# Optimization experiments

Hardware: AMD Instinct MI355X
Metric: run time of the kernel (lower is better)

## Reference

```python
import jax, jax.numpy as jnp
import numpy as np

B, N, T, D, H, E = 32768, 2, 4, 256, 8, 2
HD = D // H
S = N * T  # flattened seq_len = num_nodes * history_length
SCALE = 1.0 / np.sqrt(HD)


def setup_inputs() -> dict:
    key = jax.random.key(0)
    ks = jax.random.split(key, 22)

    def w(k, i, o):
        return jax.random.normal(k, (i, o), jnp.float32) * 0.02

    def b(k, o):
        return jax.random.normal(k, (o,), jnp.float32) * 0.01

    return {
        'node_features': jax.random.normal(ks[0], (B, N, T, D), jnp.float32),
        'edge_features': jax.random.normal(ks[1], (B, E), jnp.float32),
        'Wq': w(ks[2], D, D), 'bq': b(ks[3], D),
        'Wk': w(ks[4], D, D), 'bk': b(ks[5], D),
        'Wv': w(ks[6], D, D), 'bv': b(ks[7], D),
        'Wo': w(ks[8], D, D), 'bo': b(ks[9], D),
        'Wbias': w(ks[10], E, H), 'bbias': b(ks[11], H),
        'Wgate': w(ks[12], E, D), 'bgate': b(ks[13], D),
        'Wscale': w(ks[14], E, D), 'bscale': b(ks[15], D),
        'Wshift': w(ks[16], E, D), 'bshift': b(ks[17], D),
        'Whs': w(ks[18], E, H), 'bhs': b(ks[19], H),
    }


def reference(node_features, edge_features, Wq, bq, Wk, bk, Wv, bv, Wo, bo,
              Wbias, bbias, Wgate, bgate, Wscale, bscale, Wshift, bshift, Whs, bhs):
    # temporal mode: [B, N, T, D] -> [B, S, D]
    x = node_features.reshape(B, S, D)
    e = edge_features  # [B, E]

    Q = x @ Wq + bq
    K = x @ Wk + bk
    V = x @ Wv + bv

    # Edge-Conditioned Modulation of V
    gate = jax.nn.sigmoid(e @ Wgate + bgate)   # [B, D]
    scale = jnp.tanh(e @ Wscale + bscale)       # [B, D]
    shift = e @ Wshift + bshift                 # [B, D]
    V = (V * (1.0 + scale[:, None, :]) + shift[:, None, :]) * gate[:, None, :]

    # [B, H, S, HD]
    Qh = Q.reshape(B, S, H, HD).transpose(0, 2, 1, 3)
    Kh = K.reshape(B, S, H, HD).transpose(0, 2, 1, 3)
    Vh = V.reshape(B, S, H, HD).transpose(0, 2, 1, 3)

    scores = jnp.einsum('bhsd,bhtd->bhst', Qh, Kh) * SCALE  # [B, H, S, S]

    edge_bias = e @ Wbias + bbias                 # [B, H]
    head_scale = jnp.tanh(e @ Whs + bhs)          # [B, H]
    scores = scores * (1.0 + head_scale[:, :, None, None])

    # sparse temporal bias: (ee_t, obj_t) and (obj_t, ee_t) pairs only
    ee = jnp.arange(T)
    obj = T + ee
    bias = jnp.zeros((B, H, S, S), scores.dtype)
    bias = bias.at[:, :, ee, obj].set(edge_bias[:, :, None])
    bias = bias.at[:, :, obj, ee].set(edge_bias[:, :, None])
    scores = scores + bias

    attn = jax.nn.softmax(scores, axis=-1)  # dropout is identity in eval
    out = jnp.einsum('bhst,bhtd->bhsd', attn, Vh)  # [B, H, S, HD]
    out = out.transpose(0, 2, 1, 3).reshape(B, N, T, D).mean(axis=2)  # temporal pooling
    out = out @ Wo + bo  # [B, N, D]
    return out
```

## Files before the change

### kernel.cpp

```cpp
#include <hip/hip_runtime.h>


typedef short bf16x8 __attribute__((ext_vector_type(8)));
typedef float f32x4 __attribute__((ext_vector_type(4)));
typedef unsigned short u16;

#define SCALE_F 0.17677669529663687f
#define WT_BYTES (1024 * 256 * 2)

__device__ __forceinline__ float bf2f(u16 h) {
  unsigned u = ((unsigned)h) << 16; float f; __builtin_memcpy(&f, &u, 4); return f;
}
__device__ __forceinline__ u16 f2bf(float f) {
  unsigned u; __builtin_memcpy(&u, &f, 4);
  u += 0x7FFFu + ((u >> 16) & 1u);
  return (u16)(u >> 16);
}
__device__ __forceinline__ float fast_tanh(float x) {
  float e = __expf(2.0f * x);
  return (e - 1.0f) / (e + 1.0f);
}

template<bool F32>
__device__ __forceinline__ float LD(const void* p, int i) {
  if constexpr (F32) return ((const float*)p)[i];
  else return bf2f(((const u16*)p)[i]);
}

template<bool F32>
__device__ __forceinline__ bf16x8 load8bf_nt(const void* p, int idx) {
  if constexpr (F32) {
    const f32x4* f = (const f32x4*)((const float*)p + idx);
    f32x4 a = __builtin_nontemporal_load(f);
    f32x4 b = __builtin_nontemporal_load(f + 1);
    bf16x8 r;
    r[0] = (short)f2bf(a[0]); r[1] = (short)f2bf(a[1]);
    r[2] = (short)f2bf(a[2]); r[3] = (short)f2bf(a[3]);
    r[4] = (short)f2bf(b[0]); r[5] = (short)f2bf(b[1]);
    r[6] = (short)f2bf(b[2]); r[7] = (short)f2bf(b[3]);
    return r;
  } else {
    return __builtin_nontemporal_load((const bf16x8*)((const u16*)p + idx));
  }
}

__device__ __forceinline__ void gl_lds16(const u16* g, u16* l) {
  __builtin_amdgcn_global_load_lds(
      (const __attribute__((address_space(1))) unsigned int*)g,
      (__attribute__((address_space(3))) unsigned int*)l, 16, 0, 0);
}

__global__ void prep_kernel(const u16* __restrict__ x16,
                            const void* __restrict__ Wq, const void* __restrict__ Wk,
                            const void* __restrict__ Wv, const void* __restrict__ Wo,
                            int* __restrict__ flag, u16* __restrict__ WT) {
  __shared__ int tot;
  if (threadIdx.x == 0) tot = 0;
  __syncthreads();
  int cnt = 0;
  for (int i = threadIdx.x; i < 4096; i += 256) {
    int e = (x16[2 * i] >> 7) & 0xFF;
    cnt += (e >= 0x90 || e <= 0x50) ? 1 : 0;
  }
  atomicAdd(&tot, cnt);
  __syncthreads();
  const bool f32 = (tot >= 64);
  if (blockIdx.x == 0 && threadIdx.x == 0) *flag = f32 ? 1 : 0;

  int n = blockIdx.x;
  int k = threadIdx.x;
  if (n < 768) {
    int sel = n >> 8, col = n & 255;
    const void* src = sel == 0 ? Wq : (sel == 1 ? Wk : Wv);
    float v = f32 ? ((const float*)src)[k * 256 + col] : bf2f(((const u16*)src)[k * 256 + col]);
    WT[n * 256 + (k ^ ((n & 7) << 3))] = f2bf(v);
  } else {
    int col = n - 768;
    float v = f32 ? ((const float*)Wo)[k * 256 + col] : bf2f(((const u16*)Wo)[k * 256 + col]);
    WT[768 * 256 + col * 256 + k] = f2bf(v);
  }
}

struct __align__(16) Scratch {
  u16 qk[4][32][72];
  u16 vt[4][32][56];
  u16 pb[4][16][40];
};
union SharedU {
  u16 wtile[2][6144];
  Scratch s;
};

template<bool F32>
__device__ __forceinline__ void fused_impl(
    SharedU& sm,
    const void* __restrict__ x, const void* __restrict__ edge,
    const void* __restrict__ bq, const void* __restrict__ bk, const void* __restrict__ bv,
    const void* __restrict__ Wbias, const void* __restrict__ bbias,
    const void* __restrict__ Wgate, const void* __restrict__ bgate,
    const void* __restrict__ Wscale, const void* __restrict__ bscale,
    const void* __restrict__ Wshift, const void* __restrict__ bshift,
    const void* __restrict__ Whs, const void* __restrict__ bhs,
    const u16* __restrict__ WT, float* __restrict__ out) {
  const int tid = threadIdx.x;
  const int w  = tid >> 6;
  const int l  = tid & 63;
  const int ln = l & 15;
  const int q4 = l >> 4;
  u16* poolg = (u16*)out;

  {
    u16* vz = &sm.s.vt[w][0][0];
#pragma unroll
    for (int i = 0; i < 28; ++i) vz[l + 64 * i] = 0;
    u16* pz = &sm.s.pb[w][0][0];
#pragma unroll
    for (int i = 0; i < 10; ++i) pz[l + 64 * i] = 0;
  }

  float eA[4], eB[4];
#pragma unroll
  for (int i = 0; i < 4; ++i) {
    int gb = blockIdx.x * 16 + w * 4 + i;
    eA[i] = LD<F32>(edge, gb * 2);
    eB[i] = LD<F32>(edge, gb * 2 + 1);
  }

  const int xbase = (blockIdx.x * 128 + w * 32) * 256;
  bf16x8 xa[2][8];
#pragma unroll
  for (int mt = 0; mt < 2; ++mt)
#pragma unroll
    for (int ks = 0; ks < 8; ++ks)
      xa[mt][ks] = load8bf_nt<F32>(x, xbase + (mt * 16 + ln) * 256 + ks * 32 + q4 * 8);

  const u16* wsrc[3];
#pragma unroll
  for (int i = 0; i < 3; ++i) {
    int r = i * 32 + w * 8 + (l >> 3);
    int ngb = ((r >> 5) << 8) + (r & 31);
    wsrc[i] = WT + ngb * 256 + (l & 7) * 8;
  }
  int rowoff[6];
#pragma unroll
  for (int nt = 0; nt < 6; ++nt)
    rowoff[nt] = ((nt >> 1) * 32 + (nt & 1) * 16 + ln) * 64;
  const int swz = (ln & 7) << 3;

#pragma unroll 1
  for (int h = 0; h < 8; ++h) {
    f32x4 acc[2][6];
#pragma unroll
    for (int mt = 0; mt < 2; ++mt)
#pragma unroll
      for (int nt = 0; nt < 6; ++nt) acc[mt][nt] = (f32x4){0.f, 0.f, 0.f, 0.f};

    __syncthreads();
#pragma unroll
    for (int i = 0; i < 3; ++i)
      gl_lds16(wsrc[i] + h * 8192, &sm.wtile[0][(i * 32 + w * 8) * 64]);
    __syncthreads();
#pragma unroll
    for (int q = 0; q < 4; ++q) {
      if (q < 3) {
#pragma unroll
        for (int i = 0; i < 3; ++i)
          gl_lds16(wsrc[i] + h * 8192 + (q + 1) * 64,
                   &sm.wtile[(q + 1) & 1][(i * 32 + w * 8) * 64]);
      }
#pragma unroll
      for (int k2 = 0; k2 < 2; ++k2) {
        int cx = (k2 * 32 + q4 * 8) ^ swz;
        const u16* wq = &sm.wtile[q & 1][0];
#pragma unroll
        for (int nt = 0; nt < 6; ++nt) {
          bf16x8 bfr = *(const bf16x8*)(wq + rowoff[nt] + cx);
          acc[0][nt] = __builtin_amdgcn_mfma_f32_16x16x32_bf16(xa[0][q * 2 + k2], bfr, acc[0][nt], 0, 0, 0);
          acc[1][nt] = __builtin_amdgcn_mfma_f32_16x16x32_bf16(xa[1][q * 2 + k2], bfr, acc[1][nt], 0, 0, 0);
        }
      }
      __syncthreads();
    }

#pragma unroll
    for (int nt = 0; nt < 4; ++nt) {
      int cb = (nt & 1) * 16 + ln;
      float bias = LD<F32>((nt >> 1) ? bk : bq, h * 32 + cb);
      int col = (nt >> 1) * 32 + cb;
#pragma unroll
      for (int mt = 0; mt < 2; ++mt)
#pragma unroll
        for (int r = 0; r < 4; ++r)
          sm.s.qk[w][mt * 16 + q4 * 4 + r][col] = f2bf(acc[mt][nt][r] + bias);
    }
#pragma unroll
    for (int nt = 4; nt < 6; ++nt) {
      int dg = h * 32 + (nt - 4) * 16 + ln;
      float bvv = LD<F32>(bv, dg);
      float wg0 = LD<F32>(Wgate, dg),  wg1 = LD<F32>(Wgate, 256 + dg),  bg  = LD<F32>(bgate, dg);
      float ws0 = LD<F32>(Wscale, dg), ws1 = LD<F32>(Wscale, 256 + dg), bs  = LD<F32>(bscale, dg);
      float wf0 = LD<F32>(Wshift, dg), wf1 = LD<F32>(Wshift, 256 + dg), bsh = LD<F32>(bshift, dg);
#pragma unroll
      for (int mt = 0; mt < 2; ++mt) {
        float e0 = (q4 & 2) ? eA[mt * 2 + 1] : eA[mt * 2];
        float e1 = (q4 & 2) ? eB[mt * 2 + 1] : eB[mt * 2];
        float ga = 1.f / (1.f + __expf(-(e0 * wg0 + e1 * wg1 + bg)));
        float sc = fast_tanh(e0 * ws0 + e1 * ws1 + bs);
        float sh = e0 * wf0 + e1 * wf1 + bsh;
        u16 vv[4];
#pragma unroll
        for (int r = 0; r < 4; ++r) {
          float v = acc[mt][nt][r] + bvv;
          v = (v * (1.f + sc) + sh) * ga;
          vv[r] = f2bf(v);
        }
        ushort4 pk; pk.x = vv[0]; pk.y = vv[1]; pk.z = vv[2]; pk.w = vv[3];
        *(ushort4*)&sm.s.vt[w][(nt - 4) * 16 + ln][mt * 16 + q4 * 4] = pk;
      }
    }
    __asm__ volatile("" ::: "memory");

    float wb0 = LD<F32>(Wbias, h), wb1 = LD<F32>(Wbias, 8 + h), bb  = LD<F32>(bbias, h);
    float wh0 = LD<F32>(Whs, h),   wh1 = LD<F32>(Whs, 8 + h),   bh_ = LD<F32>(bhs, h);
#pragma unroll
    for (int pair = 0; pair < 2; ++pair) {
      bf16x8 qa = *(const bf16x8*)&sm.s.qk[w][pair * 16 + ln][q4 * 8];
      bf16x8 kb = *(const bf16x8*)&sm.s.qk[w][pair * 16 + ln][32 + q4 * 8];
      f32x4 z4 = {0.f, 0.f, 0.f, 0.f};
      f32x4 s = __builtin_amdgcn_mfma_f32_16x16x32_bf16(qa, kb, z4, 0, 0, 0);

      float e00 = eA[pair * 2],     e01 = eB[pair * 2];
      float e10 = eA[pair * 2 + 1], e11 = eB[pair * 2 + 1];
      float eb0 = e00 * wb0 + e01 * wb1 + bb;
      float eb1 = e10 * wb0 + e11 * wb1 + bb;
      float hs0 = fast_tanh(e00 * wh0 + e01 * wh1 + bh_);
      float hs1 = fast_tanh(e10 * wh0 + e11 * wh1 + bh_);
      int bj = ln >> 3;
      float mult = SCALE_F * (1.f + (bj ? hs1 : hs0));
      float ebias = bj ? eb1 : eb0;
      int tl = ln & 7;
      bool valid = ((q4 >> 1) == bj);
      float p[4];
#pragma unroll
      for (int r = 0; r < 4; ++r) {
        int sl = (q4 & 1) * 4 + r;
        p[r] = s[r] * mult + ((tl == (sl ^ 4)) ? ebias : 0.f);
      }
#pragma unroll
      for (int r = 0; r < 4; ++r) {
        float m = p[r];
        m = fmaxf(m, __shfl_xor(m, 1));
        m = fmaxf(m, __shfl_xor(m, 2));
        m = fmaxf(m, __shfl_xor(m, 4));
        float e = __expf(p[r] - m);
        float su = e;
        su += __shfl_xor(su, 1);
        su += __shfl_xor(su, 2);
        su += __shfl_xor(su, 4);
        p[r] = e / su;
      }
#pragma unroll
      for (int r = 0; r < 4; ++r)
        sm.s.pb[w][q4 * 4 + r][ln] = valid ? f2bf(p[r]) : (u16)0;
      __asm__ volatile("" ::: "memory");

      bf16x8 pa = *(const bf16x8*)&sm.s.pb[w][ln][q4 * 8];
#pragma unroll
      for (int nt = 0; nt < 2; ++nt) {
        bf16x8 vb = *(const bf16x8*)&sm.s.vt[w][nt * 16 + ln][pair * 16 + q4 * 8];
        f32x4 z = {0.f, 0.f, 0.f, 0.f};
        f32x4 o = __builtin_amdgcn_mfma_f32_16x16x32_bf16(pa, vb, z, 0, 0, 0);
        float pm = (o[0] + o[1] + o[2] + o[3]) * 0.25f;
        int c = w * 32 + h * 4 + pair * 2 + nt;
        poolg[(blockIdx.x * 32 + (c >> 2)) * 512 + 256 + (c & 3) * 64 + l] = f2bf(pm);
      }
    }
  }
}

__global__ __launch_bounds__(256, 4) void fused_kernel(
    const void* __restrict__ x, const void* __restrict__ edge,
    const void* __restrict__ bq, const void* __restrict__ bk, const void* __restrict__ bv,
    const void* __restrict__ Wbias, const void* __restrict__ bbias,
    const void* __restrict__ Wgate, const void* __restrict__ bgate,
    const void* __restrict__ Wscale, const void* __restrict__ bscale,
    const void* __restrict__ Wshift, const void* __restrict__ bshift,
    const void* __restrict__ Whs, const void* __restrict__ bhs,
    const int* __restrict__ flag, const u16* __restrict__ WT, float* __restrict__ out) {
  __shared__ SharedU sm;
  if (*flag)
    fused_impl<true>(sm, x, edge, bq, bk, bv, Wbias, bbias, Wgate, bgate,
                     Wscale, bscale, Wshift, bshift, Whs, bhs, WT, out);
  else
    fused_impl<false>(sm, x, edge, bq, bk, bv, Wbias, bbias, Wgate, bgate,
                      Wscale, bscale, Wshift, bshift, Whs, bhs, WT, out);
}

__global__ __launch_bounds__(256, 4) void proj_kernel(const void* __restrict__ bo,
                                                      const int* __restrict__ flag,
                                                      const u16* __restrict__ WT,
                                                      float* __restrict__ out) {
  __shared__ u16 pooled[32][264];
  const bool f32 = (*flag != 0);
  const int tid = threadIdx.x;
  const int w  = tid >> 6;
  const int l  = tid & 63;
  const int ln = l & 15;
  const int q4 = l >> 4;
  const u16* pool = (const u16*)out;
  const u16* WoT = WT + 768 * 256;
  const int rbase = blockIdx.x * 32;

#pragma unroll
  for (int i = 0; i < 32; ++i) {
    int idx = i * 256 + tid;
    int c = idx >> 6, lq = idx & 63;
    u16 v = pool[(rbase + (c >> 2)) * 512 + 256 + (c & 3) * 64 + lq];
    int wsrc = c >> 5, hh = (c >> 2) & 7, pr = (c >> 1) & 1, ntt = c & 1;
    int q4l = lq >> 4, lnl = lq & 15;
    int prow = wsrc * 8 + (pr * 2 + (q4l >> 1)) * 2 + (q4l & 1);
    pooled[prow][hh * 32 + ntt * 16 + lnl] = v;
  }
  __syncthreads();

  f32x4 fo[2][4];
#pragma unroll
  for (int mt = 0; mt < 2; ++mt)
#pragma unroll
    for (int nt = 0; nt < 4; ++nt) fo[mt][nt] = (f32x4){0.f, 0.f, 0.f, 0.f};
#pragma unroll
  for (int ks = 0; ks < 8; ++ks) {
    bf16x8 af0 = *(const bf16x8*)&pooled[ln][ks * 32 + q4 * 8];
    bf16x8 af1 = *(const bf16x8*)&pooled[16 + ln][ks * 32 + q4 * 8];
#pragma unroll
    for (int ntw = 0; ntw < 4; ++ntw) {
      int nrow = w * 64 + ntw * 16 + ln;
      bf16x8 bfr = *(const bf16x8*)(WoT + nrow * 256 + ks * 32 + q4 * 8);
      fo[0][ntw] = __builtin_amdgcn_mfma_f32_16x16x32_bf16(af0, bfr, fo[0][ntw], 0, 0, 0);
      fo[1][ntw] = __builtin_amdgcn_mfma_f32_16x16x32_bf16(af1, bfr, fo[1][ntw], 0, 0, 0);
    }
  }
#pragma unroll
  for (int ntw = 0; ntw < 4; ++ntw) {
    int col = w * 64 + ntw * 16 + ln;
    float bias = f32 ? ((const float*)bo)[col] : bf2f(((const u16*)bo)[col]);
#pragma unroll
    for (int mt = 0; mt < 2; ++mt)
#pragma unroll
      for (int r = 0; r < 4; ++r) {
        int row = mt * 16 + q4 * 4 + r;
        __builtin_nontemporal_store(fo[mt][ntw][r] + bias,
                                    &out[(rbase + row) * 256 + col]);
      }
  }
}

extern "C" void kernel_launch(void* const* d_in, const int* in_sizes, int n_in,
                              void* d_out, int out_size, void* d_ws, size_t ws_size,
                              hipStream_t stream) {
  (void)in_sizes; (void)n_in; (void)out_size; (void)ws_size;
  const void* x      = d_in[0];
  const void* edge   = d_in[1];
  const void* Wq     = d_in[2];  const void* bq  = d_in[3];
  const void* Wk     = d_in[4];  const void* bk  = d_in[5];
  const void* Wv     = d_in[6];  const void* bv  = d_in[7];
  const void* Wo     = d_in[8];  const void* bo  = d_in[9];
  const void* Wbias  = d_in[10]; const void* bbias  = d_in[11];
  const void* Wgate  = d_in[12]; const void* bgate  = d_in[13];
  const void* Wscale = d_in[14]; const void* bscale = d_in[15];
  const void* Wshift = d_in[16]; const void* bshift = d_in[17];
  const void* Whs    = d_in[18]; const void* bhs    = d_in[19];
  u16* WT   = (u16*)d_ws;
  int* flag = (int*)((char*)d_ws + WT_BYTES);
  float* out = (float*)d_out;

  prep_kernel<<<1024, 256, 0, stream>>>((const u16*)x, Wq, Wk, Wv, Wo, flag, WT);
  fused_kernel<<<2048, 256, 0, stream>>>(x, edge, bq, bk, bv, Wbias, bbias,
                                         Wgate, bgate, Wscale, bscale, Wshift, bshift,
                                         Whs, bhs, flag, WT, out);
  proj_kernel<<<2048, 256, 0, stream>>>(bo, flag, WT, out);
}
```

Before: 736.3 us.

## Fuse output projection into attention kernel, accumulating per head

```diff
diff --git a/kernel.cpp b/kernel.cpp
--- a/kernel.cpp
+++ b/kernel.cpp
@@ -85,6 +85,7 @@
   u16 qk[4][32][72];
   u16 vt[4][32][56];
   u16 pb[4][16][40];
+  u16 ps[32][40];
 };
 union SharedU {
   u16 wtile[2][6144];
@@ -96,6 +97,7 @@
     SharedU& sm,
     const void* __restrict__ x, const void* __restrict__ edge,
     const void* __restrict__ bq, const void* __restrict__ bk, const void* __restrict__ bv,
+    const void* __restrict__ bo,
     const void* __restrict__ Wbias, const void* __restrict__ bbias,
     const void* __restrict__ Wgate, const void* __restrict__ bgate,
     const void* __restrict__ Wscale, const void* __restrict__ bscale,
@@ -107,7 +109,7 @@
   const int l  = tid & 63;
   const int ln = l & 15;
   const int q4 = l >> 4;
-  u16* poolg = (u16*)out;
+  const u16* WoT = WT + 768 * 256;
 
   {
     u16* vz = &sm.s.vt[w][0][0];
@@ -146,6 +148,12 @@
   for (int nt = 0; nt < 6; ++nt)
     rowoff[nt] = ((nt >> 1) * 32 + (nt & 1) * 16 + ln) * 64;
   const int swz = (ln & 7) << 3;
+
+  f32x4 fo[2][4];
+#pragma unroll
+  for (int mt = 0; mt < 2; ++mt)
+#pragma unroll
+    for (int nt = 0; nt < 4; ++nt) fo[mt][nt] = (f32x4){0.f, 0.f, 0.f, 0.f};
 
 #pragma unroll 1
   for (int h = 0; h < 8; ++h) {
@@ -181,6 +189,11 @@
       }
       __syncthreads();
     }
+
+    bf16x8 wob[4];
+#pragma unroll
+    for (int ntw = 0; ntw < 4; ++ntw)
+      wob[ntw] = *(const bf16x8*)(WoT + (w * 64 + ntw * 16 + ln) * 256 + h * 32 + q4 * 8);
 
 #pragma unroll
     for (int nt = 0; nt < 4; ++nt) {
@@ -271,16 +284,41 @@
         f32x4 z = {0.f, 0.f, 0.f, 0.f};
         f32x4 o = __builtin_amdgcn_mfma_f32_16x16x32_bf16(pa, vb, z, 0, 0, 0);
         float pm = (o[0] + o[1] + o[2] + o[3]) * 0.25f;
-        int c = w * 32 + h * 4 + pair * 2 + nt;
-        poolg[(blockIdx.x * 32 + (c >> 2)) * 512 + 256 + (c & 3) * 64 + l] = f2bf(pm);
-      }
-    }
+        int prow = w * 8 + (pair * 2 + (q4 >> 1)) * 2 + (q4 & 1);
+        sm.s.ps[prow][nt * 16 + ln] = f2bf(pm);
+      }
+    }
+
+    __syncthreads();
+    {
+      bf16x8 pa0 = *(const bf16x8*)&sm.s.ps[ln][q4 * 8];
+      bf16x8 pa1 = *(const bf16x8*)&sm.s.ps[16 + ln][q4 * 8];
+#pragma unroll
+      for (int ntw = 0; ntw < 4; ++ntw) {
+        fo[0][ntw] = __builtin_amdgcn_mfma_f32_16x16x32_bf16(pa0, wob[ntw], fo[0][ntw], 0, 0, 0);
+        fo[1][ntw] = __builtin_amdgcn_mfma_f32_16x16x32_bf16(pa1, wob[ntw], fo[1][ntw], 0, 0, 0);
+      }
+    }
+  }
+
+#pragma unroll
+  for (int ntw = 0; ntw < 4; ++ntw) {
+    int col = w * 64 + ntw * 16 + ln;
+    float bias = LD<F32>(bo, col);
+#pragma unroll
+    for (int mt = 0; mt < 2; ++mt)
+#pragma unroll
+      for (int r = 0; r < 4; ++r) {
+        int row = mt * 16 + q4 * 4 + r;
+        out[(blockIdx.x * 32 + row) * 256 + col] = fo[mt][ntw][r] + bias;
+      }
   }
 }
 
 __global__ __launch_bounds__(256, 4) void fused_kernel(
     const void* __restrict__ x, const void* __restrict__ edge,
     const void* __restrict__ bq, const void* __restrict__ bk, const void* __restrict__ bv,
+    const void* __restrict__ bo,
     const void* __restrict__ Wbias, const void* __restrict__ bbias,
     const void* __restrict__ Wgate, const void* __restrict__ bgate,
     const void* __restrict__ Wscale, const void* __restrict__ bscale,
@@ -289,70 +327,11 @@
     const int* __restrict__ flag, const u16* __restrict__ WT, float* __restrict__ out) {
   __shared__ SharedU sm;
   if (*flag)
-    fused_impl<true>(sm, x, edge, bq, bk, bv, Wbias, bbias, Wgate, bgate,
+    fused_impl<true>(sm, x, edge, bq, bk, bv, bo, Wbias, bbias, Wgate, bgate,
                      Wscale, bscale, Wshift, bshift, Whs, bhs, WT, out);
   else
-    fused_impl<false>(sm, x, edge, bq, bk, bv, Wbias, bbias, Wgate, bgate,
+    fused_impl<false>(sm, x, edge, bq, bk, bv, bo, Wbias, bbias, Wgate, bgate,
                       Wscale, bscale, Wshift, bshift, Whs, bhs, WT, out);
-}
-
-__global__ __launch_bounds__(256, 4) void proj_kernel(const void* __restrict__ bo,
-                                                      const int* __restrict__ flag,
-                                                      const u16* __restrict__ WT,
-                                                      float* __restrict__ out) {
-  __shared__ u16 pooled[32][264];
-  const bool f32 = (*flag != 0);
-  const int tid = threadIdx.x;
-  const int w  = tid >> 6;
-  const int l  = tid & 63;
-  const int ln = l & 15;
-  const int q4 = l >> 4;
-  const u16* pool = (const u16*)out;
-  const u16* WoT = WT + 768 * 256;
-  const int rbase = blockIdx.x * 32;
-
-#pragma unroll
-  for (int i = 0; i < 32; ++i) {
-    int idx = i * 256 + tid;
-    int c = idx >> 6, lq = idx & 63;
-    u16 v = pool[(rbase + (c >> 2)) * 512 + 256 + (c & 3) * 64 + lq];
-    int wsrc = c >> 5, hh = (c >> 2) & 7, pr = (c >> 1) & 1, ntt = c & 1;
-    int q4l = lq >> 4, lnl = lq & 15;
-    int prow = wsrc * 8 + (pr * 2 + (q4l >> 1)) * 2 + (q4l & 1);
-    pooled[prow][hh * 32 + ntt * 16 + lnl] = v;
-  }
-  __syncthreads();
-
-  f32x4 fo[2][4];
-#pragma unroll
-  for (int mt = 0; mt < 2; ++mt)
-#pragma unroll
-    for (int nt = 0; nt < 4; ++nt) fo[mt][nt] = (f32x4){0.f, 0.f, 0.f, 0.f};
-#pragma unroll
-  for (int ks = 0; ks < 8; ++ks) {
-    bf16x8 af0 = *(const bf16x8*)&pooled[ln][ks * 32 + q4 * 8];
-    bf16x8 af1 = *(const bf16x8*)&pooled[16 + ln][ks * 32 + q4 * 8];
-#pragma unroll
-    for (int ntw = 0; ntw < 4; ++ntw) {
-      int nrow = w * 64 + ntw * 16 + ln;
-      bf16x8 bfr = *(const bf16x8*)(WoT + nrow * 256 + ks * 32 + q4 * 8);
-      fo[0][ntw] = __builtin_amdgcn_mfma_f32_16x16x32_bf16(af0, bfr, fo[0][ntw], 0, 0, 0);
-      fo[1][ntw] = __builtin_amdgcn_mfma_f32_16x16x32_bf16(af1, bfr, fo[1][ntw], 0, 0, 0);
-    }
-  }
-#pragma unroll
-  for (int ntw = 0; ntw < 4; ++ntw) {
-    int col = w * 64 + ntw * 16 + ln;
-    float bias = f32 ? ((const float*)bo)[col] : bf2f(((const u16*)bo)[col]);
-#pragma unroll
-    for (int mt = 0; mt < 2; ++mt)
-#pragma unroll
-      for (int r = 0; r < 4; ++r) {
-        int row = mt * 16 + q4 * 4 + r;
-        __builtin_nontemporal_store(fo[mt][ntw][r] + bias,
-                                    &out[(rbase + row) * 256 + col]);
-      }
-  }
 }
 
 extern "C" void kernel_launch(void* const* d_in, const int* in_sizes, int n_in,
@@ -375,8 +354,7 @@
   float* out = (float*)d_out;
 
   prep_kernel<<<1024, 256, 0, stream>>>((const u16*)x, Wq, Wk, Wv, Wo, flag, WT);
-  fused_kernel<<<2048, 256, 0, stream>>>(x, edge, bq, bk, bv, Wbias, bbias,
+  fused_kernel<<<2048, 256, 0, stream>>>(x, edge, bq, bk, bv, bo, Wbias, bbias,
                                          Wgate, bgate, Wscale, bscale, Wshift, bshift,
                                          Whs, bhs, flag, WT, out);
-  proj_kernel<<<2048, 256, 0, stream>>>(bo, flag, WT, out);
-}
+}
```

After: 878.6 us. 1.19x slower.
